# Kernel optimization log

Measured on AMD Instinct MI355X. Metric: run time of the kernel, lower is better.

The kernel has to match this reference:

```python
import jax, jax.numpy as jnp
import numpy as np

B, L, LE = 2, 1024, 1024
NM, DM, NL = 80, 512, 8
LAYERS = NL // 2
DS, EXP, K, H = 16, 2, 4, 4
DI = EXP * DM            # 1024
DTR = (DM + 15) // 16    # dt_rank 'auto' -> 32
HD = DM // H             # 128


def setup_inputs() -> dict:
    key = jax.random.key(0)
    ks = iter(jax.random.split(key, 48))
    n = lambda shape, s=0.02: jax.random.normal(next(ks), shape, jnp.float32) * s
    return {
        "x": jax.random.normal(next(ks), (B, L, NM), jnp.float32),
        "enc_output": jax.random.normal(next(ks), (B, LE, DM), jnp.float32),
        "W_in": n((DM, NM)), "b_in": jnp.zeros((DM,), jnp.float32),
        "m_norm_w": jnp.ones((LAYERS, DM), jnp.float32),
        "m_in_w": n((LAYERS, 2 * DI, DM)),
        "m_conv_w": n((LAYERS, DI, K), 0.1),
        "m_conv_b": jnp.zeros((LAYERS, DI), jnp.float32),
        "m_xproj_w": n((LAYERS, DTR + 2 * DS, DI)),
        "m_dt_w": n((LAYERS, DI, DTR)),
        "m_dt_b": n((LAYERS, DI), 0.1),
        "m_Alog": jnp.tile(jnp.log(jnp.arange(1, DS + 1, dtype=jnp.float32))[None, None, :], (LAYERS, DI, 1)),
        "m_D": jnp.ones((LAYERS, DI), jnp.float32),
        "m_out_w": n((LAYERS, DM, DI)),
        "a_in_w": n((LAYERS, 3 * DM, DM)),
        "a_in_b": jnp.zeros((LAYERS, 3 * DM), jnp.float32),
        "a_out_w": n((LAYERS, DM, DM)),
        "a_out_b": jnp.zeros((LAYERS, DM), jnp.float32),
        "a_ln_w": jnp.ones((LAYERS, DM), jnp.float32),
        "a_ln_b": jnp.zeros((LAYERS, DM), jnp.float32),
        "normf_w": jnp.ones((DM,), jnp.float32),
        "W_out": n((NM, DM)),
    }


def rmsnorm(x, w, eps=1e-5):
    return x * jax.lax.rsqrt(jnp.mean(x * x, axis=-1, keepdims=True) + eps) * w


def layernorm(x, w, b, eps=1e-5):
    m = jnp.mean(x, axis=-1, keepdims=True)
    v = jnp.mean((x - m) ** 2, axis=-1, keepdims=True)
    return (x - m) * jax.lax.rsqrt(v + eps) * w + b


def dwconv_causal(x, w, b):
    # x: (B,L,DI), w: (DI,K) depthwise; torch Conv1d(padding=K-1)[..., :L] == left-pad K-1
    xt = jnp.transpose(x, (0, 2, 1))  # (B,DI,L)
    y = jax.lax.conv_general_dilated(xt, w[:, None, :], (1,), [(K - 1, 0)],
                                     feature_group_count=DI,
                                     dimension_numbers=("NCH", "OIH", "NCH"))
    return jnp.transpose(y, (0, 2, 1)) + b


def selective_scan_cumsum(u, delta, A, Bm, Cm, Dv):
    # mamba-tiny 'cumsum' scan. u,delta: (B,L,DI); A: (DI,DS); Bm,Cm: (B,L,DS); Dv: (DI,)
    dA = jnp.einsum("bld,dn->bldn", delta, A)
    dBu = jnp.einsum("bld,bld,bln->bldn", delta, u, Bm)
    shifted = jnp.pad(dA[:, 1:], ((0, 0), (0, 1), (0, 0), (0, 0)))
    dA_cs = jnp.exp(jnp.flip(jnp.cumsum(jnp.flip(shifted, 1), 1), 1))  # suffix-sum exp
    xs = jnp.cumsum(dBu * dA_cs, axis=1) / (dA_cs + 1e-12)
    y = jnp.einsum("bldn,bln->bld", xs, Cm)
    return y + u * Dv


def mamba_block(u, in_w, conv_w, conv_b, xproj_w, dt_w, dt_b, Alog, Dv, out_w):
    xr = u @ in_w.T                       # (B,L,2*DI)
    xm, res = xr[..., :DI], xr[..., DI:]
    xm = jax.nn.silu(dwconv_causal(xm, conv_w, conv_b))
    x_dbl = xm @ xproj_w.T                # (B,L,DTR+2*DS)
    dlt = x_dbl[..., :DTR]
    Bm = x_dbl[..., DTR:DTR + DS]
    Cm = x_dbl[..., DTR + DS:]
    delta = jax.nn.softplus(dlt @ dt_w.T + dt_b)
    A = -jnp.exp(Alog)
    y = selective_scan_cumsum(xm, delta, A, Bm, Cm, Dv)
    y = y * jax.nn.silu(res)
    return y @ out_w.T


def cross_attn_block(q_in, kv, in_w, in_b, out_w, out_b, ln_w, ln_b):
    Wq, Wk, Wv = in_w[:DM], in_w[DM:2 * DM], in_w[2 * DM:]
    bq, bk, bv = in_b[:DM], in_b[DM:2 * DM], in_b[2 * DM:]
    q = (q_in @ Wq.T + bq).reshape(B, -1, H, HD)
    k = (kv @ Wk.T + bk).reshape(B, -1, H, HD)
    v = (kv @ Wv.T + bv).reshape(B, -1, H, HD)
    scores = jnp.einsum("bqhd,bkhd->bhqk", q, k) / jnp.sqrt(jnp.float32(HD))
    attn = jax.nn.softmax(scores, axis=-1)
    o = jnp.einsum("bhqk,bkhd->bqhd", attn, v).reshape(B, -1, DM)
    o = o @ out_w.T + out_b
    return layernorm(q_in + o, ln_w, ln_b)  # dropout is identity in eval


def reference(x, enc_output, W_in, b_in, m_norm_w, m_in_w, m_conv_w, m_conv_b,
              m_xproj_w, m_dt_w, m_dt_b, m_Alog, m_D, m_out_w,
              a_in_w, a_in_b, a_out_w, a_out_b, a_ln_w, a_ln_b, normf_w, W_out):
    h = x @ W_in.T + b_in
    for i in range(LAYERS):
        h = h + mamba_block(rmsnorm(h, m_norm_w[i]), m_in_w[i], m_conv_w[i],
                            m_conv_b[i], m_xproj_w[i], m_dt_w[i], m_dt_b[i],
                            m_Alog[i], m_D[i], m_out_w[i])
        h = cross_attn_block(h, enc_output, a_in_w[i], a_in_b[i],
                             a_out_w[i], a_out_b[i], a_ln_w[i], a_ln_b[i])
    h = rmsnorm(h, normf_w)
    return h @ W_out.T
```

## Files before the change

kernel.cpp:

```cpp
#include <hip/hip_runtime.h>
#include <hip/hip_bf16.h>
#include <math.h>

typedef __hip_bfloat16 bf16;
typedef __attribute__((ext_vector_type(8))) short short8x;
typedef __attribute__((ext_vector_type(4))) float f32x4;

static constexpr int cB   = 2;
static constexpr int cL   = 1024;
static constexpr int cLE  = 1024;
static constexpr int cNM  = 80;
static constexpr int cDM  = 512;
static constexpr int cLAYERS = 4;
static constexpr int cDS  = 16;
static constexpr int cKC  = 4;
static constexpr int cH   = 4;
static constexpr int cDI  = 1024;
static constexpr int cDTR = 32;
static constexpr int cHD  = 128;

static constexpr int cNCH = 64;
static constexpr int cCHL = cL / cNCH;

#define GLL16(g, l) __builtin_amdgcn_global_load_lds( \
    (const __attribute__((address_space(1))) void*)(g), \
    (__attribute__((address_space(3))) void*)(l), 16, 0, 0)

template<int ACT, int BM, int BN>
__global__ __launch_bounds__(256)
void bgemm_kernel(const bf16* __restrict__ A, const bf16* __restrict__ W,
                  const float* __restrict__ bias, const float* __restrict__ addv,
                  float* __restrict__ Cf, bf16* __restrict__ Cb,
                  int M, int N, int Kd, int lda, int ldw, int ldcf, int ldcb, int ldadd,
                  int bdiv, long sA1, long sA2, long sW1, long sW2,
                  long sCf1, long sCf2, long sCb1, long sCb2, long sBias)
{
    constexpr int RM = BM / 32;
    constexpr int RN = BN / 32;
    const int z = blockIdx.z;
    const int i1 = z / bdiv, i2 = z % bdiv;
    A += i1 * sA1 + i2 * sA2;
    W += i1 * sW1 + i2 * sW2;
    if (bias) bias += i1 * sBias;

    const int bm = blockIdx.y * BM;
    const int bn = blockIdx.x * BN;
    const int tid = threadIdx.x;
    const int lane = tid & 63;
    const int wid = tid >> 6;
    const int wr = wid >> 1, wc = wid & 1;

    __shared__ bf16 As[BM * 32];
    __shared__ bf16 Bs[BN * 32];

    f32x4 acc[RM][RN] = {};

    const int r_in = lane >> 2;
    const int kb   = (lane & 3) * 8;
    const int hi   = lane >> 4;
    const int rc   = lane & 15;

    for (int k0 = 0; k0 < Kd; k0 += 32) {
#pragma unroll
        for (int iss = 0; iss < BM / 64; iss++) {
            const int row = wid * (BM / 4) + iss * 16 + r_in;
            int gm = bm + row; if (gm >= M) gm = M - 1;
            const bf16* ga = A + (long)gm * lda + k0 + kb;
            GLL16(ga, As + (wid * (BM / 4) + iss * 16) * 32);
        }
#pragma unroll
        for (int iss = 0; iss < BN / 64; iss++) {
            const int row = wid * (BN / 4) + iss * 16 + r_in;
            int gn = bn + row; if (gn >= N) gn = N - 1;
            const bf16* gb = W + (long)gn * ldw + k0 + kb;
            GLL16(gb, Bs + (wid * (BN / 4) + iss * 16) * 32);
        }
        asm volatile("s_waitcnt vmcnt(0)" ::: "memory");
        __syncthreads();

        short8x af[RM], bfv[RN];
#pragma unroll
        for (int i = 0; i < RM; i++)
            af[i] = *(const short8x*)(As + (wr * (BM / 2) + i * 16 + rc) * 32 + hi * 8);
#pragma unroll
        for (int j = 0; j < RN; j++)
            bfv[j] = *(const short8x*)(Bs + (wc * (BN / 2) + j * 16 + rc) * 32 + hi * 8);
#pragma unroll
        for (int i = 0; i < RM; i++)
#pragma unroll
            for (int j = 0; j < RN; j++)
                acc[i][j] = __builtin_amdgcn_mfma_f32_16x16x32_bf16(af[i], bfv[j], acc[i][j], 0, 0, 0);
        __syncthreads();
    }

    const long cfo = i1 * sCf1 + i2 * sCf2;
    const long cbo = i1 * sCb1 + i2 * sCb2;
#pragma unroll
    for (int i = 0; i < RM; i++) {
#pragma unroll
        for (int r = 0; r < 4; r++) {
            const int gm = bm + wr * (BM / 2) + i * 16 + hi * 4 + r;
            if (gm >= M) continue;
#pragma unroll
            for (int j = 0; j < RN; j++) {
                const int gn = bn + wc * (BN / 2) + j * 16 + rc;
                if (gn >= N) continue;
                float v = acc[i][j][r];
                if (bias) v += bias[gn];
                if (ACT == 1) v = (v > 20.f) ? v : log1pf(__expf(v));
                if (addv) v += addv[cfo + (long)gm * ldadd + gn];
                if (Cf) Cf[cfo + (long)gm * ldcf + gn] = v;
                if (Cb) Cb[cbo + (long)gm * ldcb + gn] = __float2bfloat16(v);
            }
        }
    }
}

static inline void bgemm(int ACT, int BM, int BN, const bf16* A, const bf16* W, const float* bias,
                         const float* addv, float* Cf, bf16* Cb,
                         int M, int N, int Kd, int lda, int ldw, int ldcf, int ldcb, int ldadd,
                         int nz, int bdiv, long sA1, long sA2, long sW1, long sW2,
                         long sCf1, long sCf2, long sCb1, long sCb2, long sBias, hipStream_t s)
{
    dim3 g((N + BN - 1) / BN, (M + BM - 1) / BM, nz), b(256);
#define BG_ARGS A, W, bias, addv, Cf, Cb, M, N, Kd, lda, ldw, ldcf, ldcb, ldadd, \
                bdiv, sA1, sA2, sW1, sW2, sCf1, sCf2, sCb1, sCb2, sBias
    if (BM == 128) {
        if (ACT == 1) bgemm_kernel<1, 128, 128><<<g, b, 0, s>>>(BG_ARGS);
        else          bgemm_kernel<0, 128, 128><<<g, b, 0, s>>>(BG_ARGS);
    } else if (BN == 128) {
        if (ACT == 1) bgemm_kernel<1, 64, 128><<<g, b, 0, s>>>(BG_ARGS);
        else          bgemm_kernel<0, 64, 128><<<g, b, 0, s>>>(BG_ARGS);
    } else {
        bgemm_kernel<0, 64, 64><<<g, b, 0, s>>>(BG_ARGS);
    }
#undef BG_ARGS
}

static inline void bgemm_plain(int ACT, int BM, int BN, const bf16* A, const bf16* W,
                               const float* bias, const float* addv, float* Cf, bf16* Cb,
                               int M, int N, int Kd, int lda, int ldw, int ldcf, int ldcb,
                               int ldadd, hipStream_t s)
{
    bgemm(ACT, BM, BN, A, W, bias, addv, Cf, Cb, M, N, Kd, lda, ldw, ldcf, ldcb, ldadd,
          1, 1, 0, 0, 0, 0, 0, 0, 0, 0, 0, s);
}

__global__ __launch_bounds__(128)
void flash_attn_kernel(const bf16* __restrict__ Qp, const bf16* __restrict__ Kp,
                       const bf16* __restrict__ VTp, bf16* __restrict__ Op, float scale)
{
    const int qt = blockIdx.x;
    const int bh = blockIdx.y;
    const int b = bh >> 2, h = bh & 3;
    const int tid = threadIdx.x;
    const int w = tid >> 6;
    const int lane = tid & 63;
    const int rc = lane & 15, hi = lane >> 4;
    const int rlo = rc & 7;

    __shared__ bf16 Qs[32 * 128];
    __shared__ bf16 Ks[64 * 128];
    __shared__ bf16 Vs[128 * 64];
    __shared__ bf16 Ps[32 * 64];

    {
        const bf16* qb = Qp + ((long)(b * cL + qt * 32)) * cDM + h * cHD;
#pragma unroll
        for (int c = 0; c < 4; c++) {
            const int row = w * 16 + c * 4 + (lane >> 4);
            const int gc = (lane & 15) ^ (row & 7);
            GLL16(qb + (long)row * cDM + gc * 8, Qs + (w * 16 + c * 4) * 128);
        }
    }
    asm volatile("s_waitcnt vmcnt(0)" ::: "memory");
    __syncthreads();

    short8x aq[4];
#pragma unroll
    for (int kk = 0; kk < 4; kk++) {
        const int sc = (kk * 4 + hi) ^ rlo;
        aq[kk] = *(const short8x*)(Qs + (w * 16 + rc) * 128 + sc * 8);
    }

    float m_r[4], l_r[4];
#pragma unroll
    for (int r = 0; r < 4; r++) { m_r[r] = -1e30f; l_r[r] = 0.f; }
    f32x4 oacc[8] = {};

    const bf16* kb0 = Kp + ((long)(b * cLE)) * (2 * cDM) + h * cHD;
    const bf16* vb0 = VTp + ((long)(b * cDM + h * cHD)) * cLE;

    for (int kt = 0; kt < 16; kt++) {
        __syncthreads();
#pragma unroll
        for (int c = 0; c < 8; c++) {
            const int row = w * 32 + c * 4 + (lane >> 4);
            const int gc = (lane & 15) ^ (row & 7);
            GLL16(kb0 + ((long)(kt * 64 + row)) * (2 * cDM) + gc * 8,
                  Ks + (w * 32 + c * 4) * 128);
        }
#pragma unroll
        for (int c = 0; c < 8; c++) {
            const int row = w * 64 + c * 8 + (lane >> 3);
            const int gc = (lane & 7) ^ (row & 7);
            GLL16(vb0 + (long)row * cLE + kt * 64 + gc * 8,
                  Vs + (w * 64 + c * 8) * 64);
        }
        asm volatile("s_waitcnt vmcnt(0)" ::: "memory");
        __syncthreads();

        f32x4 s[4] = {};
#pragma unroll
        for (int kk = 0; kk < 4; kk++) {
            const int sc = (kk * 4 + hi) ^ rlo;
#pragma unroll
            for (int j = 0; j < 4; j++) {
                short8x bk = *(const short8x*)(Ks + (j * 16 + rc) * 128 + sc * 8);
                s[j] = __builtin_amdgcn_mfma_f32_16x16x32_bf16(aq[kk], bk, s[j], 0, 0, 0);
            }
        }

        float p[4][4];
        float esc[4];
#pragma unroll
        for (int r = 0; r < 4; r++) {
            const float v0 = s[0][r] * scale, v1 = s[1][r] * scale;
            const float v2 = s[2][r] * scale, v3 = s[3][r] * scale;
            float mx = fmaxf(fmaxf(v0, v1), fmaxf(v2, v3));
            mx = fmaxf(mx, __shfl_xor(mx, 1));
            mx = fmaxf(mx, __shfl_xor(mx, 2));
            mx = fmaxf(mx, __shfl_xor(mx, 4));
            mx = fmaxf(mx, __shfl_xor(mx, 8));
            const float mn = fmaxf(m_r[r], mx);
            p[0][r] = __expf(v0 - mn);
            p[1][r] = __expf(v1 - mn);
            p[2][r] = __expf(v2 - mn);
            p[3][r] = __expf(v3 - mn);
            float rs = (p[0][r] + p[1][r]) + (p[2][r] + p[3][r]);
            rs += __shfl_xor(rs, 1);
            rs += __shfl_xor(rs, 2);
            rs += __shfl_xor(rs, 4);
            rs += __shfl_xor(rs, 8);
            esc[r] = __expf(m_r[r] - mn);
            l_r[r] = l_r[r] * esc[r] + rs;
            m_r[r] = mn;
        }
#pragma unroll
        for (int j2 = 0; j2 < 8; j2++)
#pragma unroll
            for (int r = 0; r < 4; r++)
                oacc[j2][r] *= esc[r];
#pragma unroll
        for (int j = 0; j < 4; j++)
#pragma unroll
            for (int r = 0; r < 4; r++) {
                const int q = w * 16 + hi * 4 + r;
                const int cp = (j * 2 + (rc >> 3)) ^ (q & 7);
                Ps[q * 64 + cp * 8 + (rc & 7)] = __float2bfloat16(p[j][r]);
            }
        __syncthreads();
#pragma unroll
        for (int ks = 0; ks < 2; ks++) {
            const int sc = (ks * 4 + hi) ^ rlo;
            short8x ap = *(const short8x*)(Ps + (w * 16 + rc) * 64 + sc * 8);
#pragma unroll
            for (int j2 = 0; j2 < 8; j2++) {
                short8x bv = *(const short8x*)(Vs + (j2 * 16 + rc) * 64 + sc * 8);
                oacc[j2] = __builtin_amdgcn_mfma_f32_16x16x32_bf16(ap, bv, oacc[j2], 0, 0, 0);
            }
        }
    }

    float inv[4];
#pragma unroll
    for (int r = 0; r < 4; r++) inv[r] = 1.f / l_r[r];
    bf16* ob = Op + ((long)(b * cL + qt * 32)) * cDM + h * cHD;
#pragma unroll
    for (int j2 = 0; j2 < 8; j2++)
#pragma unroll
        for (int r = 0; r < 4; r++)
            ob[(long)(w * 16 + hi * 4 + r) * cDM + j2 * 16 + rc] =
                __float2bfloat16(oacc[j2][r] * inv[r]);
}

__global__ void splitk_reduce_kernel(const float* __restrict__ parts, float* __restrict__ outf,
                                     bf16* __restrict__ outb, int n4, int sliceN4, int S)
{
    const int i = blockIdx.x * 256 + threadIdx.x;
    if (i >= n4) return;
    float4 a = ((const float4*)parts)[i];
    for (int s2 = 1; s2 < S; s2++) {
        float4 b2 = ((const float4*)parts)[i + (long)s2 * sliceN4];
        a.x += b2.x; a.y += b2.y; a.z += b2.z; a.w += b2.w;
    }
    ((float4*)outf)[i] = a;
    bf16 b0 = __float2bfloat16(a.x), b1 = __float2bfloat16(a.y);
    bf16 b2 = __float2bfloat16(a.z), b3 = __float2bfloat16(a.w);
    short4 pk = { *(short*)&b0, *(short*)&b1, *(short*)&b2, *(short*)&b3 };
    ((short4*)outb)[i] = pk;
}

__global__ void cvt_all_kernel(
    const float* __restrict__ s0, bf16* __restrict__ d0,
    const float* __restrict__ s1, bf16* __restrict__ d1,
    const float* __restrict__ s2, bf16* __restrict__ d2,
    const float* __restrict__ s3, bf16* __restrict__ d3,
    const float* __restrict__ s4, bf16* __restrict__ d4,
    const float* __restrict__ s5, bf16* __restrict__ d5,
    const float* __restrict__ s6, bf16* __restrict__ d6,
    const float* __restrict__ s7, bf16* __restrict__ d7)
{
    constexpr long E0 = 1048576, E1 = 4194304, E2 = 262144, E3 = 131072;
    constexpr long E4 = 2097152, E5 = 3145728, E6 = 1048576, E7 = 40960;
    constexpr long C0 = E0, C1 = C0 + E1, C2 = C1 + E2, C3 = C2 + E3;
    constexpr long C4 = C3 + E4, C5 = C4 + E5, C6 = C5 + E6, C7 = C6 + E7;
    long i = ((long)blockIdx.x * 256 + threadIdx.x) * 4;
    if (i >= C7) return;
    const float* s; bf16* d;
    if      (i < C0) { s = s0; d = d0; }
    else if (i < C1) { s = s1; d = d1; i -= C0; }
    else if (i < C2) { s = s2; d = d2; i -= C1; }
    else if (i < C3) { s = s3; d = d3; i -= C2; }
    else if (i < C4) { s = s4; d = d4; i -= C3; }
    else if (i < C5) { s = s5; d = d5; i -= C4; }
    else if (i < C6) { s = s6; d = d6; i -= C5; }
    else             { s = s7; d = d7; i -= C6; }
    float4 v = *(const float4*)(s + i);
    d[i]     = __float2bfloat16(v.x);
    d[i + 1] = __float2bfloat16(v.y);
    d[i + 2] = __float2bfloat16(v.z);
    d[i + 3] = __float2bfloat16(v.w);
}

__global__ void cvt_pad_kernel(const float* __restrict__ in, bf16* __restrict__ out,
                               int rows, int kin, int kout)
{
    const int idx = blockIdx.x * 256 + threadIdx.x;
    if (idx >= rows * kout) return;
    const int r = idx / kout, k = idx - r * kout;
    out[idx] = __float2bfloat16(k < kin ? in[(long)r * kin + k] : 0.f);
}

__global__ void transpose_bf16_kernel(const bf16* __restrict__ in, bf16* __restrict__ out,
                                      int ldin, int col0, long inLS, long outLS)
{
    __shared__ bf16 t[32][33];
    const int z = blockIdx.z;
    const int lay = z >> 1, b = z & 1;
    in  += (long)lay * inLS;
    out += (long)lay * outLS;
    const int le0 = blockIdx.x * 32, d0 = blockIdx.y * 32;
    const int tid = threadIdx.x;
    const int c = tid & 31, r = tid >> 5;
    for (int i = r; i < 32; i += 8)
        t[i][c] = in[((long)b * cLE + le0 + i) * ldin + col0 + d0 + c];
    __syncthreads();
    for (int i = r; i < 32; i += 8)
        out[((long)b * cDM + d0 + i) * cLE + le0 + c] = t[c][i];
}

__global__ void rmsnorm_kernel(const float* __restrict__ x, const float* __restrict__ w,
                               float* __restrict__ outf, bf16* __restrict__ outb, int Dm)
{
    const int row = blockIdx.x;
    const float* xr = x + (long)row * Dm;
    float s = 0.f;
    for (int i = threadIdx.x; i < Dm; i += 256) { float v = xr[i]; s += v * v; }
    __shared__ float red[5];
    const int lane = threadIdx.x & 63, wv = threadIdx.x >> 6;
#pragma unroll
    for (int off = 1; off < 64; off <<= 1) s += __shfl_xor(s, off);
    if (lane == 0) red[wv] = s;
    __syncthreads();
    if (threadIdx.x == 0) {
        float t = red[0] + red[1] + red[2] + red[3];
        red[4] = rsqrtf(t / Dm + 1e-5f);
    }
    __syncthreads();
    const float scale = red[4];
    for (int i = threadIdx.x; i < Dm; i += 256) {
        float v = xr[i] * scale * w[i];
        if (outf) outf[(long)row * Dm + i] = v;
        if (outb) outb[(long)row * Dm + i] = __float2bfloat16(v);
    }
}

__global__ void layernorm_kernel(const float* __restrict__ x, const float* __restrict__ w,
                                 const float* __restrict__ b, float* __restrict__ outf,
                                 bf16* __restrict__ outb, int Dm)
{
    const int row = blockIdx.x;
    const float* xr = x + (long)row * Dm;
    float s = 0.f, sq = 0.f;
    for (int i = threadIdx.x; i < Dm; i += 256) { float v = xr[i]; s += v; sq += v * v; }
    __shared__ float red[8];
    __shared__ float mv[2];
    const int lane = threadIdx.x & 63, wv = threadIdx.x >> 6;
#pragma unroll
    for (int off = 1; off < 64; off <<= 1) { s += __shfl_xor(s, off); sq += __shfl_xor(sq, off); }
    if (lane == 0) { red[wv] = s; red[4 + wv] = sq; }
    __syncthreads();
    if (threadIdx.x == 0) {
        float ts = red[0] + red[1] + red[2] + red[3];
        float tq = red[4] + red[5] + red[6] + red[7];
        float m = ts / Dm;
        float var = tq / Dm - m * m;
        mv[0] = m;
        mv[1] = rsqrtf(var + 1e-5f);
    }
    __syncthreads();
    const float m = mv[0], rs = mv[1];
    for (int i = threadIdx.x; i < Dm; i += 256) {
        float v = (xr[i] - m) * rs * w[i] + b[i];
        outf[(long)row * Dm + i] = v;
        outb[(long)row * Dm + i] = __float2bfloat16(v);
    }
}

__global__ void conv_silu_kernel(const float* __restrict__ xr, const float* __restrict__ w,
                                 const float* __restrict__ bias, float* __restrict__ xm,
                                 bf16* __restrict__ xmb)
{
    const int idx = blockIdx.x * 256 + threadIdx.x;
    if (idx >= cB * cL * cDI) return;
    const int d = idx & (cDI - 1);
    const int l = (idx >> 10) & (cL - 1);
    const int b = idx >> 20;
    float s = bias[d];
#pragma unroll
    for (int j = 0; j < cKC; j++) {
        const int ls = l + j - (cKC - 1);
        if (ls >= 0) s += w[d * cKC + j] * xr[((long)(b * cL + ls)) * (2 * cDI) + d];
    }
    s = s / (1.f + __expf(-s));
    xm[(long)idx] = s;
    xmb[(long)idx] = __float2bfloat16(s);
}

__global__ void scan_phase1(const float* __restrict__ xm, const float* __restrict__ delta,
                            const float* __restrict__ xdbl, const float* __restrict__ Alog,
                            float* __restrict__ aprod_out, float* __restrict__ send_out)
{
    const int idx4 = blockIdx.x * 256 + threadIdx.x;
    const int ng = idx4 & 3;
    const int d  = (idx4 >> 2) & (cDI - 1);
    const int ch = (idx4 >> 12) & (cNCH - 1);
    const int b  = idx4 >> 18;
    const float4 Al = *(const float4*)(Alog + d * cDS + 4 * ng);
    const float A0 = -__expf(Al.x), A1 = -__expf(Al.y), A2 = -__expf(Al.z), A3 = -__expf(Al.w);
    float s0 = 0.f, s1 = 0.f, s2 = 0.f, s3 = 0.f;
    float p0 = 1.f, p1 = 1.f, p2 = 1.f, p3 = 1.f;
    const int l0 = ch * cCHL;
    const float* dp = delta + (long)(b * cL + l0) * cDI + d;
    const float* up = xm    + (long)(b * cL + l0) * cDI + d;
    const float* xb = xdbl  + (long)(b * cL + l0) * 64 + cDTR + 4 * ng;
#pragma unroll
    for (int t = 0; t < cCHL; t++) {
        const float dl = dp[(long)t * cDI];
        const float du = dl * up[(long)t * cDI];
        const float4 Bv = *(const float4*)(xb + (long)t * 64);
        const float a0 = __expf(dl * A0), a1 = __expf(dl * A1);
        const float a2 = __expf(dl * A2), a3 = __expf(dl * A3);
        s0 = a0 * s0 + du * Bv.x; p0 *= a0;
        s1 = a1 * s1 + du * Bv.y; p1 *= a1;
        s2 = a2 * s2 + du * Bv.z; p2 *= a2;
        s3 = a3 * s3 + du * Bv.w; p3 *= a3;
    }
    const long base4 = (((long)(b * cNCH + ch) * cDI + d) * cDS) + 4 * ng;
    float4 pv = { p0, p1, p2, p3 };
    float4 sv = { s0, s1, s2, s3 };
    *(float4*)(aprod_out + base4) = pv;
    *(float4*)(send_out + base4)  = sv;
}

__global__ void scan_phase2(const float* __restrict__ aprod, const float* __restrict__ send,
                            float* __restrict__ sinit)
{
    const int j = blockIdx.x * 256 + threadIdx.x;
    const int n = j & (cDS - 1);
    const int d = (j >> 4) & (cDI - 1);
    const int b = j >> 14;
    float s = 0.f;
#pragma unroll
    for (int c = 0; c < cNCH; c++) {
        const long off = (((long)(b * cNCH + c) * cDI + d) * cDS) + n;
        sinit[off] = s;
        s = aprod[off] * s + send[off];
    }
}

__global__ void scan_phase3(const float* __restrict__ xm, const float* __restrict__ delta,
                            const float* __restrict__ xdbl, const float* __restrict__ Alog,
                            const float* __restrict__ Dv, const float* __restrict__ xr,
                            const float* __restrict__ sinit, bf16* __restrict__ y)
{
    const int idx4 = blockIdx.x * 256 + threadIdx.x;
    const int ng = idx4 & 3;
    const int d  = (idx4 >> 2) & (cDI - 1);
    const int ch = (idx4 >> 12) & (cNCH - 1);
    const int b  = idx4 >> 18;
    const float4 Al = *(const float4*)(Alog + d * cDS + 4 * ng);
    const float A0 = -__expf(Al.x), A1 = -__expf(Al.y), A2 = -__expf(Al.z), A3 = -__expf(Al.w);
    const float Dval = Dv[d];
    const long base4 = (((long)(b * cNCH + ch) * cDI + d) * cDS) + 4 * ng;
    float4 st = *(const float4*)(sinit + base4);
    float s0 = st.x, s1 = st.y, s2 = st.z, s3 = st.w;
    const int l0 = ch * cCHL;
    const float* dp = delta + (long)(b * cL + l0) * cDI + d;
    const float* up = xm    + (long)(b * cL + l0) * cDI + d;
    const float* xb = xdbl  + (long)(b * cL + l0) * 64 + cDTR + 4 * ng;
    const float* xc = xb + cDS;
    const float* rp = xr + (long)(b * cL + l0) * (2 * cDI) + cDI + d;
    bf16* yp = y + (long)(b * cL + l0) * cDI + d;
#pragma unroll
    for (int t = 0; t < cCHL; t++) {
        const float dl = dp[(long)t * cDI];
        const float u  = up[(long)t * cDI];
        const float du = dl * u;
        const float4 Bv = *(const float4*)(xb + (long)t * 64);
        const float4 Cv = *(const float4*)(xc + (long)t * 64);
        const float a0 = __expf(dl * A0), a1 = __expf(dl * A1);
        const float a2 = __expf(dl * A2), a3 = __expf(dl * A3);
        s0 = a0 * s0 + du * Bv.x;
        s1 = a1 * s1 + du * Bv.y;
        s2 = a2 * s2 + du * Bv.z;
        s3 = a3 * s3 + du * Bv.w;
        float c = s0 * Cv.x;
        c = fmaf(s1, Cv.y, c);
        c = fmaf(s2, Cv.z, c);
        c = fmaf(s3, Cv.w, c);
        c += __shfl_xor(c, 1);
        c += __shfl_xor(c, 2);
        if (ng == 0) {
            const float res = rp[(long)t * 2 * cDI];
            const float sig = 1.f / (1.f + __expf(-res));
            yp[(long)t * cDI] = __float2bfloat16((c + u * Dval) * (res * sig));
        }
    }
}

extern "C" void kernel_launch(void* const* d_in, const int* in_sizes, int n_in,
                              void* d_out, int out_size, void* d_ws, size_t ws_size,
                              hipStream_t stream)
{
    const float* x       = (const float*)d_in[0];
    const float* enc     = (const float*)d_in[1];
    const float* W_in    = (const float*)d_in[2];
    const float* b_in    = (const float*)d_in[3];
    const float* m_norm_w= (const float*)d_in[4];
    const float* m_in_w  = (const float*)d_in[5];
    const float* m_conv_w= (const float*)d_in[6];
    const float* m_conv_b= (const float*)d_in[7];
    const float* m_xproj = (const float*)d_in[8];
    const float* m_dt_w  = (const float*)d_in[9];
    const float* m_dt_b  = (const float*)d_in[10];
    const float* m_Alog  = (const float*)d_in[11];
    const float* m_D     = (const float*)d_in[12];
    const float* m_out_w = (const float*)d_in[13];
    const float* a_in_w  = (const float*)d_in[14];
    const float* a_in_b  = (const float*)d_in[15];
    const float* a_out_w = (const float*)d_in[16];
    const float* a_out_b = (const float*)d_in[17];
    const float* a_ln_w  = (const float*)d_in[18];
    const float* a_ln_b  = (const float*)d_in[19];
    const float* normf_w = (const float*)d_in[20];
    const float* W_out   = (const float*)d_in[21];
    float* out = (float*)d_out;

    float* ws = (float*)d_ws;
    long off = 0;
    auto allocf = [&](long n) { float* p = ws + off; off += n; return p; };

    const long M1 = 1 << 20;
    float* bufH    = allocf(M1);
    float* bufPre  = allocf(M1);
    float* bufXR   = allocf(4 * M1);
    float* bufXM   = allocf(2 * M1);
    float* bufDelta= allocf(2 * M1);
    float* bufXDBL = allocf(M1 / 8);
    bf16* bufU    = (bf16*)allocf(M1 / 2);
    bf16* bufHb   = (bf16*)allocf(M1 / 2);
    bf16* bufXMb  = (bf16*)allocf(M1);
    bf16* bufXDBLb= (bf16*)allocf(M1 / 16);
    bf16* bufY    = (bf16*)allocf(M1);
    bf16* bufQ    = (bf16*)allocf(M1 / 2);
    bf16* bufO    = (bf16*)allocf(M1 / 2);
    bf16* encb    = (bf16*)allocf(M1 / 2);
    bf16* w_in_b  = (bf16*)allocf(2 * M1);
    bf16* w_xp_b  = (bf16*)allocf(M1 / 8);
    bf16* w_dt_b  = (bf16*)allocf(M1 / 16);
    bf16* w_out_b = (bf16*)allocf(M1);
    bf16* w_ain_b = (bf16*)allocf(3 * M1 / 2);
    bf16* w_aout_b= (bf16*)allocf(M1 / 2);
    bf16* x_pad   = (bf16*)allocf(2048L * 96 / 2);
    bf16* w_inp_b = (bf16*)allocf(512L * 96 / 2);
    bf16* w_outf_b= (bf16*)allocf(80L * 512 / 2);
    float* bufAP  = allocf(2 * M1);
    float* bufSE  = allocf(2 * M1);
    float* bufSI  = allocf(2 * M1);
    bf16* bufKV4  = (bf16*)allocf(4 * M1);
    bf16* bufVT4  = (bf16*)allocf(2 * M1);

    const int Mrows = cB * cL;
    const long SUMSZ4 = (long)cB * cNCH * cDI * 4;
    const long kvLS = (long)Mrows * 2 * cDM;
    const long vtLS = (long)cB * cDM * cLE;

    cvt_all_kernel<<<11688, 256, 0, stream>>>(
        enc, encb, m_in_w, w_in_b, m_xproj, w_xp_b, m_dt_w, w_dt_b,
        m_out_w, w_out_b, a_in_w, w_ain_b, a_out_w, w_aout_b, W_out, w_outf_b);
    cvt_pad_kernel<<<(Mrows * 96 + 255) / 256, 256, 0, stream>>>(x, x_pad, Mrows, cNM, 96);
    cvt_pad_kernel<<<(cDM * 96 + 255) / 256, 256, 0, stream>>>(W_in, w_inp_b, cDM, cNM, 96);

    bgemm(0, 64, 128, encb, w_ain_b + (long)cDM * cDM, a_in_b + cDM, nullptr, nullptr, bufKV4,
          Mrows, 2 * cDM, cDM, cDM, cDM, 0, 2 * cDM, 0,
          cLAYERS, 1,
          0, 0,
          (long)3 * cDM * cDM, 0,
          0, 0, kvLS, 0,
          (long)3 * cDM,
          stream);
    {
        dim3 g(cLE / 32, cDM / 32, cLAYERS * cB);
        transpose_bf16_kernel<<<g, 256, 0, stream>>>(bufKV4, bufVT4, 2 * cDM, cDM, kvLS, vtLS);
    }

    bgemm_plain(0, 64, 64, x_pad, w_inp_b, b_in, nullptr, bufH, nullptr,
                Mrows, cDM, 96, 96, 96, cDM, 0, 0, stream);

    for (int i = 0; i < cLAYERS; i++) {
        const float* norm_w = m_norm_w + (long)i * cDM;
        const bf16*  in_w   = w_in_b   + (long)i * 2 * cDI * cDM;
        const float* conv_w = m_conv_w + (long)i * cDI * cKC;
        const float* conv_b = m_conv_b + (long)i * cDI;
        const bf16*  xproj  = w_xp_b   + (long)i * 64 * cDI;
        const bf16*  dt_w   = w_dt_b   + (long)i * cDI * cDTR;
        const float* dt_b   = m_dt_b   + (long)i * cDI;
        const float* Alog   = m_Alog   + (long)i * cDI * cDS;
        const float* Dv     = m_D      + (long)i * cDI;
        const bf16*  out_w  = w_out_b  + (long)i * cDM * cDI;
        const bf16*  ain_w  = w_ain_b  + (long)i * 3 * cDM * cDM;
        const float* ain_b  = a_in_b   + (long)i * 3 * cDM;
        const bf16*  aout_w = w_aout_b + (long)i * cDM * cDM;
        const float* aout_b = a_out_b  + (long)i * cDM;
        const float* ln_w   = a_ln_w   + (long)i * cDM;
        const float* ln_b   = a_ln_b   + (long)i * cDM;
        const bf16*  kv_l   = bufKV4 + (long)i * kvLS;
        const bf16*  vt_l   = bufVT4 + (long)i * vtLS;

        rmsnorm_kernel<<<Mrows, 256, 0, stream>>>(bufH, norm_w, nullptr, bufU, cDM);
        bgemm_plain(0, 64, 128, bufU, in_w, nullptr, nullptr, bufXR, nullptr,
                    Mrows, 2 * cDI, cDM, cDM, cDM, 2 * cDI, 0, 0, stream);
        conv_silu_kernel<<<(cB * cL * cDI) / 256, 256, 0, stream>>>(bufXR, conv_w, conv_b, bufXM, bufXMb);
        bgemm(0, 64, 64, bufXMb, xproj, nullptr, nullptr, bufPre, nullptr,
              Mrows, 64, cDI / 8, cDI, cDI, 64, 0, 0,
              8, 1, 128, 0, 128, 0, (long)Mrows * 64, 0, 0, 0, 0, stream);
        splitk_reduce_kernel<<<(Mrows * 64 / 4 + 255) / 256, 256, 0, stream>>>(
            bufPre, bufXDBL, bufXDBLb, Mrows * 64 / 4, Mrows * 64 / 4, 8);
        bgemm_plain(1, 64, 128, bufXDBLb, dt_w, dt_b, nullptr, bufDelta, nullptr,
                    Mrows, cDI, cDTR, 64, cDTR, cDI, 0, 0, stream);
        scan_phase1<<<(int)(SUMSZ4 / 256), 256, 0, stream>>>(bufXM, bufDelta, bufXDBL, Alog, bufAP, bufSE);
        scan_phase2<<<(cB * cDI * cDS) / 256, 256, 0, stream>>>(bufAP, bufSE, bufSI);
        scan_phase3<<<(int)(SUMSZ4 / 256), 256, 0, stream>>>(bufXM, bufDelta, bufXDBL, Alog, Dv, bufXR, bufSI, bufY);
        bgemm_plain(0, 64, 64, bufY, out_w, nullptr, bufH, bufH, bufHb,
                    Mrows, cDM, cDI, cDI, cDI, cDM, cDM, cDM, stream);

        bgemm_plain(0, 64, 64, bufHb, ain_w, ain_b, nullptr, nullptr, bufQ,
                    Mrows, cDM, cDM, cDM, cDM, 0, cDM, 0, stream);
        {
            dim3 g(cL / 32, cB * cH);
            flash_attn_kernel<<<g, 128, 0, stream>>>(bufQ, kv_l, vt_l, bufO,
                                                     0.08838834764831845f);
        }
        bgemm_plain(0, 64, 64, bufO, aout_w, aout_b, bufH, bufPre, nullptr,
                    Mrows, cDM, cDM, cDM, cDM, cDM, 0, cDM, stream);
        layernorm_kernel<<<Mrows, 256, 0, stream>>>(bufPre, ln_w, ln_b, bufH, bufHb, cDM);
    }

    rmsnorm_kernel<<<Mrows, 256, 0, stream>>>(bufH, normf_w, nullptr, bufU, cDM);
    bgemm_plain(0, 64, 64, bufU, w_outf_b, nullptr, nullptr, out, nullptr,
                Mrows, cNM, cDM, cDM, cDM, cNM, 0, 0, stream);
}
```

Baseline: 797.4 us.

## Fuse Q projection into flash attention and RMSNorm into layernorm epilogue

The flash attention kernel now computes the per-head Q projection itself with MFMA over the bf16 hidden state and Wq, staging tiles in the K/V shared buffers. This removes the separate Q GEMM launch and its bufQ round trip. The layernorm kernel additionally computes the next layer's RMSNorm (or the final norm) so the standalone rmsnorm launches go away. scan_phase2 now uses 64-thread blocks for more blocks. Each attention block recomputes Q for its 32 rows with a serialized k-loop, and this adds sync overhead.

```diff
diff --git a/kernel.cpp b/kernel.cpp
--- a/kernel.cpp
+++ b/kernel.cpp
@@ -147,8 +147,10 @@
 }
 
 __global__ __launch_bounds__(128)
-void flash_attn_kernel(const bf16* __restrict__ Qp, const bf16* __restrict__ Kp,
-                       const bf16* __restrict__ VTp, bf16* __restrict__ Op, float scale)
+void flash_attn_kernel(const bf16* __restrict__ Hb, const bf16* __restrict__ Wq,
+                       const float* __restrict__ bq,
+                       const bf16* __restrict__ Kp, const bf16* __restrict__ VTp,
+                       bf16* __restrict__ Op, float scale)
 {
     const int qt = blockIdx.x;
     const int bh = blockIdx.y;
@@ -158,6 +160,8 @@
     const int lane = tid & 63;
     const int rc = lane & 15, hi = lane >> 4;
     const int rlo = rc & 7;
+    const int r_in = lane >> 2;
+    const int kb   = (lane & 3) * 8;
 
     __shared__ bf16 Qs[32 * 128];
     __shared__ bf16 Ks[64 * 128];
@@ -165,15 +169,39 @@
     __shared__ bf16 Ps[32 * 64];
 
     {
-        const bf16* qb = Qp + ((long)(b * cL + qt * 32)) * cDM + h * cHD;
-#pragma unroll
-        for (int c = 0; c < 4; c++) {
-            const int row = w * 16 + c * 4 + (lane >> 4);
-            const int gc = (lane & 15) ^ (row & 7);
-            GLL16(qb + (long)row * cDM + gc * 8, Qs + (w * 16 + c * 4) * 128);
-        }
-    }
-    asm volatile("s_waitcnt vmcnt(0)" ::: "memory");
+        bf16* HsT = Vs;
+        bf16* WsT = Ks;
+        const bf16* hb0 = Hb + ((long)(b * cL + qt * 32)) * cDM;
+        const bf16* wq0 = Wq + (long)h * cHD * cDM;
+        f32x4 qacc[8] = {};
+        for (int k0 = 0; k0 < cDM; k0 += 32) {
+            __syncthreads();
+            GLL16(hb0 + (long)(w * 16 + r_in) * cDM + k0 + kb, HsT + (w * 16) * 32);
+#pragma unroll
+            for (int iss = 0; iss < 4; iss++)
+                GLL16(wq0 + (long)(iss * 32 + w * 16 + r_in) * cDM + k0 + kb,
+                      WsT + (iss * 32 + w * 16) * 32);
+            asm volatile("s_waitcnt vmcnt(0)" ::: "memory");
+            __syncthreads();
+            short8x aH = *(const short8x*)(HsT + (w * 16 + rc) * 32 + hi * 8);
+#pragma unroll
+            for (int j = 0; j < 8; j++) {
+                short8x bW = *(const short8x*)(WsT + (j * 16 + rc) * 32 + hi * 8);
+                qacc[j] = __builtin_amdgcn_mfma_f32_16x16x32_bf16(aH, bW, qacc[j], 0, 0, 0);
+            }
+        }
+        __syncthreads();
+#pragma unroll
+        for (int j2 = 0; j2 < 8; j2++)
+#pragma unroll
+            for (int r = 0; r < 4; r++) {
+                const int qrow = w * 16 + hi * 4 + r;
+                const int col = j2 * 16 + rc;
+                const float qv = qacc[j2][r] + bq[h * cHD + col];
+                Qs[qrow * 128 + (((col >> 3) ^ (qrow & 7)) << 3) + (col & 7)] =
+                    __float2bfloat16(qv);
+            }
+    }
     __syncthreads();
 
     short8x aq[4];
@@ -388,34 +416,48 @@
 
 __global__ void layernorm_kernel(const float* __restrict__ x, const float* __restrict__ w,
                                  const float* __restrict__ b, float* __restrict__ outf,
-                                 bf16* __restrict__ outb, int Dm)
+                                 bf16* __restrict__ outb,
+                                 const float* __restrict__ rms_w, bf16* __restrict__ rms_out)
 {
     const int row = blockIdx.x;
-    const float* xr = x + (long)row * Dm;
-    float s = 0.f, sq = 0.f;
-    for (int i = threadIdx.x; i < Dm; i += 256) { float v = xr[i]; s += v; sq += v * v; }
+    const float* xr = x + (long)row * 512;
+    const int t = threadIdx.x;
+    const int i0 = t, i1 = t + 256;
+    float x0 = xr[i0], x1 = xr[i1];
+    float s = x0 + x1, sq = x0 * x0 + x1 * x1;
     __shared__ float red[8];
     __shared__ float mv[2];
-    const int lane = threadIdx.x & 63, wv = threadIdx.x >> 6;
+    const int lane = t & 63, wv = t >> 6;
 #pragma unroll
     for (int off = 1; off < 64; off <<= 1) { s += __shfl_xor(s, off); sq += __shfl_xor(sq, off); }
     if (lane == 0) { red[wv] = s; red[4 + wv] = sq; }
     __syncthreads();
-    if (threadIdx.x == 0) {
+    if (t == 0) {
         float ts = red[0] + red[1] + red[2] + red[3];
         float tq = red[4] + red[5] + red[6] + red[7];
-        float m = ts / Dm;
-        float var = tq / Dm - m * m;
+        float m = ts / 512.f;
+        float var = tq / 512.f - m * m;
         mv[0] = m;
         mv[1] = rsqrtf(var + 1e-5f);
     }
     __syncthreads();
     const float m = mv[0], rs = mv[1];
-    for (int i = threadIdx.x; i < Dm; i += 256) {
-        float v = (xr[i] - m) * rs * w[i] + b[i];
-        outf[(long)row * Dm + i] = v;
-        outb[(long)row * Dm + i] = __float2bfloat16(v);
-    }
+    const float v0 = (x0 - m) * rs * w[i0] + b[i0];
+    const float v1 = (x1 - m) * rs * w[i1] + b[i1];
+    outf[(long)row * 512 + i0] = v0;
+    outf[(long)row * 512 + i1] = v1;
+    outb[(long)row * 512 + i0] = __float2bfloat16(v0);
+    outb[(long)row * 512 + i1] = __float2bfloat16(v1);
+    float s2 = v0 * v0 + v1 * v1;
+#pragma unroll
+    for (int off = 1; off < 64; off <<= 1) s2 += __shfl_xor(s2, off);
+    if (lane == 0) red[wv] = s2;
+    __syncthreads();
+    if (t == 0) mv[0] = rsqrtf((red[0] + red[1] + red[2] + red[3]) / 512.f + 1e-5f);
+    __syncthreads();
+    const float rsc = mv[0];
+    rms_out[(long)row * 512 + i0] = __float2bfloat16(v0 * rsc * rms_w[i0]);
+    rms_out[(long)row * 512 + i1] = __float2bfloat16(v1 * rsc * rms_w[i1]);
 }
 
 __global__ void conv_silu_kernel(const float* __restrict__ xr, const float* __restrict__ w,
@@ -477,7 +519,7 @@
 __global__ void scan_phase2(const float* __restrict__ aprod, const float* __restrict__ send,
                             float* __restrict__ sinit)
 {
-    const int j = blockIdx.x * 256 + threadIdx.x;
+    const int j = blockIdx.x * 64 + threadIdx.x;
     const int n = j & (cDS - 1);
     const int d = (j >> 4) & (cDI - 1);
     const int b = j >> 14;
@@ -584,7 +626,6 @@
     bf16* bufXMb  = (bf16*)allocf(M1);
     bf16* bufXDBLb= (bf16*)allocf(M1 / 16);
     bf16* bufY    = (bf16*)allocf(M1);
-    bf16* bufQ    = (bf16*)allocf(M1 / 2);
     bf16* bufO    = (bf16*)allocf(M1 / 2);
     bf16* encb    = (bf16*)allocf(M1 / 2);
     bf16* w_in_b  = (bf16*)allocf(2 * M1);
@@ -628,9 +669,9 @@
 
     bgemm_plain(0, 64, 64, x_pad, w_inp_b, b_in, nullptr, bufH, nullptr,
                 Mrows, cDM, 96, 96, 96, cDM, 0, 0, stream);
+    rmsnorm_kernel<<<Mrows, 256, 0, stream>>>(bufH, m_norm_w, nullptr, bufU, cDM);
 
     for (int i = 0; i < cLAYERS; i++) {
-        const float* norm_w = m_norm_w + (long)i * cDM;
         const bf16*  in_w   = w_in_b   + (long)i * 2 * cDI * cDM;
         const float* conv_w = m_conv_w + (long)i * cDI * cKC;
         const float* conv_b = m_conv_b + (long)i * cDI;
@@ -648,8 +689,8 @@
         const float* ln_b   = a_ln_b   + (long)i * cDM;
         const bf16*  kv_l   = bufKV4 + (long)i * kvLS;
         const bf16*  vt_l   = bufVT4 + (long)i * vtLS;
-
-        rmsnorm_kernel<<<Mrows, 256, 0, stream>>>(bufH, norm_w, nullptr, bufU, cDM);
+        const float* next_rms_w = (i + 1 < cLAYERS) ? (m_norm_w + (long)(i + 1) * cDM) : normf_w;
+
         bgemm_plain(0, 64, 128, bufU, in_w, nullptr, nullptr, bufXR, nullptr,
                     Mrows, 2 * cDI, cDM, cDM, cDM, 2 * cDI, 0, 0, stream);
         conv_silu_kernel<<<(cB * cL * cDI) / 256, 256, 0, stream>>>(bufXR, conv_w, conv_b, bufXM, bufXMb);
@@ -661,24 +702,22 @@
         bgemm_plain(1, 64, 128, bufXDBLb, dt_w, dt_b, nullptr, bufDelta, nullptr,
                     Mrows, cDI, cDTR, 64, cDTR, cDI, 0, 0, stream);
         scan_phase1<<<(int)(SUMSZ4 / 256), 256, 0, stream>>>(bufXM, bufDelta, bufXDBL, Alog, bufAP, bufSE);
-        scan_phase2<<<(cB * cDI * cDS) / 256, 256, 0, stream>>>(bufAP, bufSE, bufSI);
+        scan_phase2<<<(cB * cDI * cDS) / 64, 64, 0, stream>>>(bufAP, bufSE, bufSI);
         scan_phase3<<<(int)(SUMSZ4 / 256), 256, 0, stream>>>(bufXM, bufDelta, bufXDBL, Alog, Dv, bufXR, bufSI, bufY);
         bgemm_plain(0, 64, 64, bufY, out_w, nullptr, bufH, bufH, bufHb,
                     Mrows, cDM, cDI, cDI, cDI, cDM, cDM, cDM, stream);
 
-        bgemm_plain(0, 64, 64, bufHb, ain_w, ain_b, nullptr, nullptr, bufQ,
-                    Mrows, cDM, cDM, cDM, cDM, 0, cDM, 0, stream);
         {
             dim3 g(cL / 32, cB * cH);
-            flash_attn_kernel<<<g, 128, 0, stream>>>(bufQ, kv_l, vt_l, bufO,
+            flash_attn_kernel<<<g, 128, 0, stream>>>(bufHb, ain_w, ain_b, kv_l, vt_l, bufO,
                                                      0.08838834764831845f);
         }
         bgemm_plain(0, 64, 64, bufO, aout_w, aout_b, bufH, bufPre, nullptr,
                     Mrows, cDM, cDM, cDM, cDM, cDM, 0, cDM, stream);
-        layernorm_kernel<<<Mrows, 256, 0, stream>>>(bufPre, ln_w, ln_b, bufH, bufHb, cDM);
-    }
-
-    rmsnorm_kernel<<<Mrows, 256, 0, stream>>>(bufH, normf_w, nullptr, bufU, cDM);
+        layernorm_kernel<<<Mrows, 256, 0, stream>>>(bufPre, ln_w, ln_b, bufH, bufHb,
+                                                    next_rms_w, bufU);
+    }
+
     bgemm_plain(0, 64, 64, bufU, w_outf_b, nullptr, nullptr, out, nullptr,
                 Mrows, cNM, cDM, cDM, cDM, cNM, 0, 0, stream);
 }
```

Result: faster. 770.3 us (-3.4%).
